# Optimization experiments

Measured on AMD Instinct MI355X. Metric: run time of the kernel, lower is better.

## Reference

```python
import jax, jax.numpy as jnp
import numpy as np

B, L, D, FF = 4, 4096, 1024, 4096
EPS = 1e-06


def setup_inputs() -> dict:
    key = jax.random.key(0)
    ks = jax.random.split(key, 20)
    s_d = 1.0 / np.sqrt(D)
    s_ff = 1.0 / np.sqrt(FF)
    inp = {
        "x": jax.random.normal(ks[0], (B, L, D), jnp.float32),
        "hidden": jax.random.normal(ks[1], (B, D), jnp.float32),
        # sioconv linears (stored as [in, out])
        "w_ln_z": jax.random.normal(ks[2], (D, D), jnp.float32) * s_d,
        "b_ln_z": jnp.zeros((D,), jnp.float32),
        "w_dt": jax.random.normal(ks[3], (D, D), jnp.float32) * s_d,
        "b_dt": jnp.zeros((D,), jnp.float32),
        "w_y": jax.random.normal(ks[4], (D, D), jnp.float32) * s_d,
        "b_y": jnp.zeros((D,), jnp.float32),
        "w_y_act": jax.random.normal(ks[5], (D, D), jnp.float32) * s_d,
        "b_y_act": jnp.zeros((D,), jnp.float32),
        # FFN SwiGLU
        "w_fc": jax.random.normal(ks[6], (D, FF), jnp.float32) * s_d,
        "b_fc": jnp.zeros((FF,), jnp.float32),
        "w_fc_act": jax.random.normal(ks[7], (D, FF), jnp.float32) * s_d,
        "b_fc_act": jnp.zeros((FF,), jnp.float32),
        "w_out": jax.random.normal(ks[8], (FF, D), jnp.float32) * s_ff,
        "b_out": jnp.zeros((D,), jnp.float32),
        # RMSNorm gains
        "g_sio": jnp.ones((D,), jnp.float32),
        "g_ffn": jnp.ones((D,), jnp.float32),
    }
    return inp


def _rmsnorm(x, g):
    return x * jax.lax.rsqrt(jnp.mean(x * x, axis=-1, keepdims=True) + EPS) * g


def _sioconv(x, hidden, w_ln_z, b_ln_z, w_dt, b_dt, w_y, b_y, w_y_act, b_y_act):
    # x: [B,L,D], hidden: [B,D]
    ln_z = -jax.nn.softplus(-(x @ w_ln_z + b_ln_z))       # [B,L,D]
    dt = x @ w_dt + b_dt
    ln_da = -jax.nn.softplus(-dt)
    ln_o_da = -jax.nn.softplus(dt)
    ln_o_da_cumsum = jnp.cumsum(ln_o_da, axis=1)
    # inner-chunk: exp(logcumsumexp(ln_z + ln_da - cumsum) + cumsum)
    lse = jax.lax.cumlogsumexp(ln_z + ln_da - ln_o_da_cumsum, axis=1)
    h_inner = jnp.exp(lse + ln_o_da_cumsum)
    # cross-chunk: decay applied to incoming hidden state
    h_cross = jnp.exp(ln_o_da_cumsum) * hidden[:, None, :]
    h = h_inner + h_cross
    y = (h @ w_y + b_y) * jax.nn.silu(x @ w_y_act + b_y_act)
    return y, h


def _ffn(x, w_fc, b_fc, w_fc_act, b_fc_act, w_out, b_out):
    return (x @ w_fc + b_fc) * jax.nn.silu(x @ w_fc_act + b_fc_act) @ w_out + b_out


def reference(x, hidden, w_ln_z, b_ln_z, w_dt, b_dt, w_y, b_y, w_y_act, b_y_act,
              w_fc, b_fc, w_fc_act, b_fc_act, w_out, b_out, g_sio, g_ffn):
    x_res = x
    y, h = _sioconv(_rmsnorm(x, g_sio), hidden,
                    w_ln_z, b_ln_z, w_dt, b_dt, w_y, b_y, w_y_act, b_y_act)
    x = y + x_res  # dropout is identity (p=0 / eval)
    x_res = x
    x = _ffn(_rmsnorm(x, g_ffn), w_fc, b_fc, w_fc_act, b_fc_act, w_out, b_out) + x_res
    return (x, h)
```

## Files before the change

### kernel.cpp

```cpp
#include <hip/hip_runtime.h>
#include <stdint.h>

using u16 = unsigned short;
typedef __attribute__((ext_vector_type(8))) __bf16 bf16x8;
typedef __attribute__((ext_vector_type(4))) float f32x4;

#define DEV __device__ __forceinline__

static constexpr int kB = 4, kL = 4096, kD = 1024, kFF = 4096;
static constexpr int kM = kB * kL;
static constexpr int kLC = 256, kNC = kL / kLC;
static constexpr float kEPS = 1e-6f;

DEV u16 f2bf(float v) {
  union { float f; uint32_t u; } x; x.f = v;
  uint32_t r = x.u + 0x7FFFu + ((x.u >> 16) & 1u);
  return (u16)(r >> 16);
}
DEV float bf2f(u16 u) {
  union { uint32_t u; float f; } x; x.u = (uint32_t)u << 16; return x.f;
}
DEV float sigm(float x) { return 1.0f / (1.0f + __expf(-x)); }

DEV void gload_lds16(const void* g, void* l) {
  __builtin_amdgcn_global_load_lds(
      (const __attribute__((address_space(1))) void*)g,
      (__attribute__((address_space(3))) void*)l, 16, 0, 0);
}

__global__ __launch_bounds__(256) void wtrans_all(
    const float* __restrict__ w_ln_z, const float* __restrict__ w_dt,
    const float* __restrict__ w_fca, const float* __restrict__ w_fc,
    const float* __restrict__ w_yact, const float* __restrict__ w_y,
    const float* __restrict__ w_out_,
    u16* __restrict__ wzdT, u16* __restrict__ wfgT, u16* __restrict__ wyaT,
    u16* __restrict__ wyT, u16* __restrict__ woutT) {
  const int bid = blockIdx.x;
  const float *a, *b; u16* out; int K, Ncols, bx, local; bool pair;
  if (bid < 2048)       { local = bid;         a = w_ln_z; b = w_dt; out = wzdT;  K = 1024; Ncols = 1024; bx = 64;  pair = true;  }
  else if (bid < 10240) { local = bid - 2048;  a = w_fca;  b = w_fc; out = wfgT;  K = 1024; Ncols = 4096; bx = 256; pair = true;  }
  else if (bid < 11264) { local = bid - 10240; a = w_yact; b = nullptr; out = wyaT; K = 1024; Ncols = 1024; bx = 32; pair = false; }
  else if (bid < 12288) { local = bid - 11264; a = w_y;    b = nullptr; out = wyT;  K = 1024; Ncols = 1024; bx = 32; pair = false; }
  else                  { local = bid - 12288; a = w_out_; b = nullptr; out = woutT; K = 4096; Ncols = 1024; bx = 32; pair = false; }
  const int n0 = (local % bx) * 32, k0 = (local / bx) * 32;
  __shared__ float t[32][33];
  const int tx = threadIdx.x, ty = threadIdx.y;
  const float* src; int c0;
  if (pair) { src = ((n0 >> 5) & 1) ? b : a; c0 = (n0 >> 6) * 32; }
  else      { src = a; c0 = n0; }
#pragma unroll
  for (int i = 0; i < 4; ++i)
    t[ty + i * 8][tx] = src[(size_t)(k0 + ty + i * 8) * Ncols + (c0 + tx)];
  __syncthreads();
#pragma unroll
  for (int i = 0; i < 4; ++i)
    out[(size_t)(n0 + ty + i * 8) * K + (k0 + tx)] = f2bf(t[tx][ty + i * 8]);
}

__global__ __launch_bounds__(256) void rmsnorm_kernel(const float* __restrict__ x,
                                                      const float* __restrict__ g,
                                                      u16* __restrict__ out) {
  const int row = blockIdx.x;
  const int t = threadIdx.x;
  const float4 v = ((const float4*)(x + (size_t)row * kD))[t];
  float ss = v.x * v.x + v.y * v.y + v.z * v.z + v.w * v.w;
#pragma unroll
  for (int o = 1; o < 64; o <<= 1) ss += __shfl_xor(ss, o, 64);
  __shared__ float red[4];
  if ((t & 63) == 0) red[t >> 6] = ss;
  __syncthreads();
  const float tot = red[0] + red[1] + red[2] + red[3];
  const float sc = rsqrtf(tot * (1.0f / kD) + kEPS);
  const float4 gv = ((const float4*)g)[t];
  const uint32_t lo = (uint32_t)f2bf(v.x * sc * gv.x) | ((uint32_t)f2bf(v.y * sc * gv.y) << 16);
  const uint32_t hi = (uint32_t)f2bf(v.z * sc * gv.z) | ((uint32_t)f2bf(v.w * sc * gv.w) << 16);
  *(uint2*)(out + (size_t)row * kD + t * 4) = make_uint2(lo, hi);
}

__global__ __launch_bounds__(256) void rmsnorm_b16(const u16* __restrict__ x,
                                                   const float* __restrict__ g,
                                                   u16* __restrict__ out) {
  const int row = blockIdx.x;
  const int t = threadIdx.x;
  const uint2 raw = ((const uint2*)(x + (size_t)row * kD))[t];
  const float v0 = bf2f((u16)(raw.x & 0xffff)), v1 = bf2f((u16)(raw.x >> 16));
  const float v2 = bf2f((u16)(raw.y & 0xffff)), v3 = bf2f((u16)(raw.y >> 16));
  float ss = v0 * v0 + v1 * v1 + v2 * v2 + v3 * v3;
#pragma unroll
  for (int o = 1; o < 64; o <<= 1) ss += __shfl_xor(ss, o, 64);
  __shared__ float red[4];
  if ((t & 63) == 0) red[t >> 6] = ss;
  __syncthreads();
  const float tot = red[0] + red[1] + red[2] + red[3];
  const float sc = rsqrtf(tot * (1.0f / kD) + kEPS);
  const float4 gv = ((const float4*)g)[t];
  const uint32_t lo = (uint32_t)f2bf(v0 * sc * gv.x) | ((uint32_t)f2bf(v1 * sc * gv.y) << 16);
  const uint32_t hi = (uint32_t)f2bf(v2 * sc * gv.z) | ((uint32_t)f2bf(v3 * sc * gv.w) << 16);
  *(uint2*)(out + (size_t)row * kD + t * 4) = make_uint2(lo, hi);
}

template <int MODE>
__global__ __launch_bounds__(512) void gemm256(
    const u16* __restrict__ A, const u16* __restrict__ Bt,
    const float* __restrict__ bias, const float* __restrict__ bias2,
    const u16* __restrict__ aux, int auxld,
    const float* __restrict__ res, float* __restrict__ Cf,
    u16* __restrict__ Cb, u16* __restrict__ C2b,
    float* __restrict__ Pg, float* __restrict__ Sg,
    int M, int N, int K) {
  __shared__ u16 sm[65536];
  const int tid = threadIdx.x;
  const int lane = tid & 63;
  const int wave = tid >> 6;
  const int wr = wave >> 2, wc = wave & 3;

  const int gx = gridDim.x;
  const int nwg = gx * gridDim.y;
  const int bid = blockIdx.y * gx + blockIdx.x;
  const int q = nwg >> 3, r = nwg & 7;
  const int xcd = bid & 7, idx0 = bid >> 3;
  const int wg = (xcd < r ? xcd * (q + 1) : r * (q + 1) + (xcd - r) * q) + idx0;
  const int m0 = (wg / gx) * 256, n0 = (wg % gx) * 256;

  const int NK = K >> 6;

  const int l8 = lane >> 3, l7 = lane & 7;
  const int rsub = wave * 8 + l8;
  const int kel = (l7 ^ l8) * 8;
  const size_t srcA = (size_t)(m0 + rsub) * K + kel;
  const size_t srcB = (size_t)(n0 + rsub) * K + kel;

  auto stage_half = [&](int kt, int half) {
    const int bsel = (kt & 1) * 32768;
    if (half < 2) {
      u16* d = sm + bsel + tid * 8 + half * 8192;
      const u16* s = A + srcA + (size_t)kt * 64 + (size_t)(half * 2) * 64 * K;
      gload_lds16(s, d);
      gload_lds16(s + (size_t)64 * K, d + 4096);
    } else {
      const int hh = half - 2;
      u16* d = sm + bsel + 16384 + tid * 8 + hh * 8192;
      const u16* s = Bt + srcB + (size_t)kt * 64 + (size_t)(hh * 2) * 64 * K;
      gload_lds16(s, d);
      gload_lds16(s + (size_t)64 * K, d + 4096);
    }
  };

  const int ra = lane & 15;
  const int kx0 = ((lane >> 4) ^ l7) * 8;
  const int kx1 = (((lane >> 4) + 4) ^ l7) * 8;

  f32x4 acc[8][4] = {};
  bf16x8 al[4][2], ah[4][2], bl[2][2], bh[2][2];

  stage_half(0, 0); stage_half(0, 1); stage_half(0, 2); stage_half(0, 3);
  stage_half(1, 0);
  asm volatile("s_waitcnt vmcnt(2)");
  asm volatile("s_barrier" ::: "memory");

  for (int h = 0; h < NK; ++h) {
    const u16* as = sm + (h & 1) * 32768 + (wr * 128 + ra) * 64;
    const u16* bs = sm + (h & 1) * 32768 + 16384 + (wc * 64 + ra) * 64;

#pragma unroll
    for (int mi = 0; mi < 4; ++mi) {
      al[mi][0] = *(const bf16x8*)(as + mi * 16 * 64 + kx0);
      al[mi][1] = *(const bf16x8*)(as + mi * 16 * 64 + kx1);
    }
#pragma unroll
    for (int ni = 0; ni < 2; ++ni) {
      bl[ni][0] = *(const bf16x8*)(bs + ni * 16 * 64 + kx0);
      bl[ni][1] = *(const bf16x8*)(bs + ni * 16 * 64 + kx1);
    }
    if (h + 1 < NK) stage_half(h + 1, 1);
    asm volatile("s_barrier" ::: "memory");
    asm volatile("s_waitcnt lgkmcnt(0)");
    __builtin_amdgcn_s_setprio(1);
#pragma unroll
    for (int mi = 0; mi < 4; ++mi)
#pragma unroll
      for (int ni = 0; ni < 2; ++ni)
#pragma unroll
        for (int kk = 0; kk < 2; ++kk)
          acc[mi][ni] = __builtin_amdgcn_mfma_f32_16x16x32_bf16(al[mi][kk], bl[ni][kk], acc[mi][ni], 0, 0, 0);
    __builtin_amdgcn_s_setprio(0);
    asm volatile("s_barrier" ::: "memory");

#pragma unroll
    for (int ni = 0; ni < 2; ++ni) {
      bh[ni][0] = *(const bf16x8*)(bs + (32 + ni * 16) * 64 + kx0);
      bh[ni][1] = *(const bf16x8*)(bs + (32 + ni * 16) * 64 + kx1);
    }
    if (h + 1 < NK) stage_half(h + 1, 2);
    asm volatile("s_barrier" ::: "memory");
    asm volatile("s_waitcnt lgkmcnt(0)");
    __builtin_amdgcn_s_setprio(1);
#pragma unroll
    for (int mi = 0; mi < 4; ++mi)
#pragma unroll
      for (int ni = 0; ni < 2; ++ni)
#pragma unroll
        for (int kk = 0; kk < 2; ++kk)
          acc[mi][2 + ni] = __builtin_amdgcn_mfma_f32_16x16x32_bf16(al[mi][kk], bh[ni][kk], acc[mi][2 + ni], 0, 0, 0);
    __builtin_amdgcn_s_setprio(0);
    asm volatile("s_barrier" ::: "memory");

#pragma unroll
    for (int mi = 0; mi < 4; ++mi) {
      ah[mi][0] = *(const bf16x8*)(as + (64 + mi * 16) * 64 + kx0);
      ah[mi][1] = *(const bf16x8*)(as + (64 + mi * 16) * 64 + kx1);
    }
    if (h + 1 < NK) stage_half(h + 1, 3);
    asm volatile("s_barrier" ::: "memory");
    asm volatile("s_waitcnt lgkmcnt(0)");
    __builtin_amdgcn_s_setprio(1);
#pragma unroll
    for (int mi = 0; mi < 4; ++mi)
#pragma unroll
      for (int ni = 0; ni < 2; ++ni)
#pragma unroll
        for (int kk = 0; kk < 2; ++kk)
          acc[4 + mi][ni] = __builtin_amdgcn_mfma_f32_16x16x32_bf16(ah[mi][kk], bl[ni][kk], acc[4 + mi][ni], 0, 0, 0);
    __builtin_amdgcn_s_setprio(0);
    asm volatile("s_barrier" ::: "memory");

    if (h + 2 < NK) stage_half(h + 2, 0);
    asm volatile("s_barrier" ::: "memory");
    __builtin_amdgcn_s_setprio(1);
#pragma unroll
    for (int mi = 0; mi < 4; ++mi)
#pragma unroll
      for (int ni = 0; ni < 2; ++ni)
#pragma unroll
        for (int kk = 0; kk < 2; ++kk)
          acc[4 + mi][2 + ni] = __builtin_amdgcn_mfma_f32_16x16x32_bf16(ah[mi][kk], bh[ni][kk], acc[4 + mi][2 + ni], 0, 0, 0);
    __builtin_amdgcn_s_setprio(0);
    if (h + 2 < NK) asm volatile("s_waitcnt vmcnt(2)");
    else            asm volatile("s_waitcnt vmcnt(0)");
    asm volatile("s_barrier" ::: "memory");
  }

  const int ca = ra;
  const int rq = (lane >> 4) * 4;
  if (MODE == 7) {
    const int Nout = N >> 1;
    float Pacc[2] = {1.f, 1.f}, Sacc[2] = {0.f, 0.f};
#pragma unroll
    for (int mi = 0; mi < 8; ++mi) {
#pragma unroll
      for (int ni = 0; ni < 2; ++ni) {
        const int cout = (n0 >> 1) + wc * 32 + ni * 16 + ca;
        const float b1 = bias[cout], b2 = bias2[cout];
        float pj = 1.f, sj = 0.f;
#pragma unroll
        for (int j = 0; j < 4; ++j) {
          const int rr = m0 + wr * 128 + mi * 16 + rq + j;
          const size_t idx = (size_t)rr * Nout + cout;
          const float v1 = acc[mi][ni][j] + b1;
          const float v2 = acc[mi][2 + ni][j] + b2;
          const float Aa = sigm(-v2);
          const float Bb = sigm(v1) * sigm(v2);
          Cf[idx] = Aa;
          C2b[idx] = f2bf(Bb);
          pj *= Aa;
          sj = fmaf(Aa, sj, Bb);
        }
        float P16 = 1.f, S16 = 0.f;
#pragma unroll
        for (int qq = 0; qq < 4; ++qq) {
          const float pq = __shfl(pj, ca + qq * 16, 64);
          const float sq = __shfl(sj, ca + qq * 16, 64);
          P16 *= pq;
          S16 = fmaf(pq, S16, sq);
        }
        Sacc[ni] = fmaf(P16, Sacc[ni], S16);
        Pacc[ni] *= P16;
      }
    }
    float* smF = (float*)sm;
    __syncthreads();
    if ((lane >> 4) == 0) {
#pragma unroll
      for (int ni = 0; ni < 2; ++ni) {
        const int col = wc * 32 + ni * 16 + ca;
        smF[wr * 128 + col] = Pacc[ni];
        smF[256 + wr * 128 + col] = Sacc[ni];
      }
    }
    __syncthreads();
    if (wr == 0 && (lane >> 4) == 0) {
      const int bb = m0 >> 12, cc = (m0 & 4095) >> 8;
#pragma unroll
      for (int ni = 0; ni < 2; ++ni) {
        const int col = wc * 32 + ni * 16 + ca;
        const float P0 = smF[col],       P1 = smF[128 + col];
        const float S0 = smF[256 + col], S1 = smF[256 + 128 + col];
        const size_t o = ((size_t)bb * kNC + cc) * kD + ((n0 >> 1) + col);
        Pg[o] = P0 * P1;
        Sg[o] = fmaf(P1, S0, S1);
      }
    }
  } else {
#pragma unroll
    for (int mi = 0; mi < 8; ++mi) {
#pragma unroll
      for (int ni = 0; ni < 4; ++ni) {
        const int c = n0 + wc * 64 + ni * 16 + ca;
        const float bz = bias[c];
#pragma unroll
        for (int j = 0; j < 4; ++j) {
          const int rr = m0 + wr * 128 + mi * 16 + rq + j;
          const size_t idx = (size_t)rr * N + c;
          const float v = acc[mi][ni][j] + bz;
          if (MODE == 2) {
            const float a = bf2f(aux[(size_t)rr * auxld + c]);
            Cb[idx] = f2bf(v * (a * sigm(a)) + res[idx]);
          } else if (MODE == 8) {
            Cf[idx] = v + bf2f(aux[(size_t)rr * auxld + c]);
          } else {
            Cb[idx] = f2bf(v);
          }
        }
      }
    }
  }
}

__global__ __launch_bounds__(512, 4) void gemm_ffn(
    const u16* __restrict__ A, const u16* __restrict__ Bt,
    const float* __restrict__ bias, const float* __restrict__ bias2,
    u16* __restrict__ Cb, int M, int N, int K) {
  __shared__ u16 sm[24576];
  const int tid = threadIdx.x;
  const int lane = tid & 63;
  const int wave = tid >> 6;
  const int wr = wave >> 1, wc = wave & 1;

  const int gx = gridDim.x;
  const int nwg = gx * gridDim.y;
  const int bid = blockIdx.y * gx + blockIdx.x;
  const int q = nwg >> 3, r = nwg & 7;
  const int xcd = bid & 7, idx0 = bid >> 3;
  const int wg = (xcd < r ? xcd * (q + 1) : r * (q + 1) + (xcd - r) * q) + idx0;
  const int per = gridDim.y * 4;
  const int sg = wg / per, srem = wg % per;
  const int m0 = (srem >> 2) * 256;
  const int n0 = (sg * 4 + (srem & 3)) * 128;

  const int NK = K >> 5;

  const int rsub = wave * 16 + (lane >> 2);
  const int kel = ((lane & 3) ^ ((lane >> 3) & 3)) * 8;
  const size_t srcA = (size_t)(m0 + rsub) * K + kel;
  const size_t srcB = (size_t)(n0 + rsub) * K + kel;

  auto stageA = [&](int kt) {
    u16* d = sm + (kt & 1) * 12288 + tid * 8;
    const u16* s = A + srcA + (size_t)kt * 32;
    gload_lds16(s, d);
    gload_lds16(s + (size_t)128 * K, d + 4096);
  };
  auto stageB = [&](int kt) {
    gload_lds16(Bt + srcB + (size_t)kt * 32,
                sm + (kt & 1) * 12288 + 8192 + tid * 8);
  };

  const int ra = lane & 15;
  const int rb = ra * 32 + ((((lane >> 4) ^ (ra >> 1)) & 3) << 3);

  f32x4 acc[4][4] = {};
  bf16x8 af[4], bfr[4];

  stageA(0); stageB(0);
  if (NK > 1) { stageA(1); stageB(1); }
  asm volatile("s_waitcnt vmcnt(3)");
  asm volatile("s_barrier" ::: "memory");

  for (int h = 0; h < NK; ++h) {
    const u16* Az = sm + (h & 1) * 12288 + wr * 2048;
    const u16* Bz = sm + (h & 1) * 12288 + 8192 + wc * 2048;

#pragma unroll
    for (int mi = 0; mi < 4; ++mi) af[mi] = *(const bf16x8*)(Az + mi * 512 + rb);
    bfr[0] = *(const bf16x8*)(Bz + rb);
    bfr[1] = *(const bf16x8*)(Bz + 512 + rb);
    asm volatile("s_barrier" ::: "memory");
    asm volatile("s_waitcnt lgkmcnt(0)");
    __builtin_amdgcn_s_setprio(1);
#pragma unroll
    for (int mi = 0; mi < 4; ++mi)
#pragma unroll
      for (int ni = 0; ni < 2; ++ni)
        acc[mi][ni] = __builtin_amdgcn_mfma_f32_16x16x32_bf16(af[mi], bfr[ni], acc[mi][ni], 0, 0, 0);
    __builtin_amdgcn_s_setprio(0);
    asm volatile("s_barrier" ::: "memory");

    bfr[2] = *(const bf16x8*)(Bz + 1024 + rb);
    bfr[3] = *(const bf16x8*)(Bz + 1536 + rb);
    if (h + 2 < NK) stageA(h + 2);
    asm volatile("s_barrier" ::: "memory");
    asm volatile("s_waitcnt lgkmcnt(0)");
    __builtin_amdgcn_s_setprio(1);
#pragma unroll
    for (int mi = 0; mi < 4; ++mi)
      acc[mi][2] = __builtin_amdgcn_mfma_f32_16x16x32_bf16(af[mi], bfr[2], acc[mi][2], 0, 0, 0);
    __builtin_amdgcn_s_setprio(0);
    asm volatile("s_barrier" ::: "memory");

    if (h + 2 < NK) stageB(h + 2);
    __builtin_amdgcn_s_setprio(1);
#pragma unroll
    for (int mi = 0; mi < 4; ++mi)
      acc[mi][3] = __builtin_amdgcn_mfma_f32_16x16x32_bf16(af[mi], bfr[3], acc[mi][3], 0, 0, 0);
    __builtin_amdgcn_s_setprio(0);
    if (h + 2 < NK) asm volatile("s_waitcnt vmcnt(3)");
    else            asm volatile("s_waitcnt vmcnt(0)");
    asm volatile("s_barrier" ::: "memory");
  }

  const int ca = lane & 15;
  const int rq = (lane >> 4) * 4;
  const int Nout = N >> 1;
#pragma unroll
  for (int mi = 0; mi < 4; ++mi) {
#pragma unroll
    for (int ni = 0; ni < 2; ++ni) {
      const int cout = (n0 >> 1) + wc * 32 + ni * 16 + ca;
      const float b1 = bias[cout], b2 = bias2[cout];
#pragma unroll
      for (int j = 0; j < 4; ++j) {
        const int rr = m0 + wr * 64 + mi * 16 + rq + j;
        const size_t idx = (size_t)rr * Nout + cout;
        const float v1 = acc[mi][ni][j] + b1;
        const float v2 = acc[mi][2 + ni][j] + b2;
        Cb[idx] = f2bf(v2 * (v1 * sigm(v1)));
      }
    }
  }
}

__global__ __launch_bounds__(256) void scan_phase2(const float* __restrict__ P,
                                                   const float* __restrict__ S,
                                                   const float* __restrict__ hidden,
                                                   float* __restrict__ Hini) {
  const int d = blockIdx.x * 256 + threadIdx.x;
  const int b = blockIdx.y;
  float carry = hidden[(size_t)b * kD + d];
  for (int c = 0; c < kNC; ++c) {
    const size_t o = ((size_t)b * kNC + c) * kD + d;
    Hini[o] = carry;
    carry = fmaf(P[o], carry, S[o]);
  }
}

__global__ __launch_bounds__(256) void scan_phase3(const float* __restrict__ Aa,
                                                   const u16* __restrict__ Bv,
                                                   const float* __restrict__ Hini,
                                                   float* __restrict__ Hout,
                                                   u16* __restrict__ Hbf) {
  const int d = blockIdx.x * 256 + threadIdx.x;
  const int c = blockIdx.y, b = blockIdx.z;
  float h = Hini[((size_t)b * kNC + c) * kD + d];
  size_t base = ((size_t)b * kL + (size_t)c * kLC) * kD + d;
#pragma unroll 4
  for (int l = 0; l < kLC; ++l) {
    h = fmaf(Aa[base], h, bf2f(Bv[base]));
    Hout[base] = h;
    Hbf[base] = f2bf(h);
    base += kD;
  }
}

extern "C" void kernel_launch(void* const* d_in, const int* in_sizes, int n_in,
                              void* d_out, int out_size, void* d_ws, size_t ws_size,
                              hipStream_t stream) {
  const float* x      = (const float*)d_in[0];
  const float* hidden = (const float*)d_in[1];
  const float* w_ln_z = (const float*)d_in[2];
  const float* b_ln_z = (const float*)d_in[3];
  const float* w_dt   = (const float*)d_in[4];
  const float* b_dt   = (const float*)d_in[5];
  const float* w_y    = (const float*)d_in[6];
  const float* b_y    = (const float*)d_in[7];
  const float* w_yact = (const float*)d_in[8];
  const float* b_yact = (const float*)d_in[9];
  const float* w_fc   = (const float*)d_in[10];
  const float* b_fc   = (const float*)d_in[11];
  const float* w_fca  = (const float*)d_in[12];
  const float* b_fca  = (const float*)d_in[13];
  const float* w_out  = (const float*)d_in[14];
  const float* b_out  = (const float*)d_in[15];
  const float* g_sio  = (const float*)d_in[16];
  const float* g_ffn  = (const float*)d_in[17];

  char* ws = (char*)d_ws;
  const size_t MiB = 1ull << 20;
  u16* wzdT  = (u16*)(ws + 0 * MiB);
  u16* wyaT  = (u16*)(ws + 4 * MiB);
  u16* wyT   = (u16*)(ws + 6 * MiB);
  u16* wfgT  = (u16*)(ws + 8 * MiB);
  u16* woutT = (u16*)(ws + 24 * MiB);
  u16*   xn    = (u16*)(ws + 33 * MiB);
  u16*   yabuf = (u16*)(ws + 65 * MiB);
  float* Abuf  = (float*)(ws + 97 * MiB);
  u16*   x1b   = (u16*)(ws + 97 * MiB);
  u16*   Bvbuf = (u16*)(ws + 161 * MiB);
  u16*   hbf   = (u16*)(ws + 225 * MiB);
  u16*   Ubuf  = (u16*)(ws + 161 * MiB);
  float* Pbuf  = (float*)(ws + 289 * MiB);
  float* Sbuf  = (float*)(ws + 290 * MiB);
  float* Hini  = (float*)(ws + 291 * MiB);

  float* xout = (float*)d_out;
  float* hout = xout + (size_t)kM * kD;

  wtrans_all<<<16384, dim3(32, 8), 0, stream>>>(
      w_ln_z, w_dt, w_fca, w_fc, w_yact, w_y, w_out,
      wzdT, wfgT, wyaT, wyT, woutT);

  rmsnorm_kernel<<<kM, 256, 0, stream>>>(x, g_sio, xn);

  gemm256<7><<<dim3(2048 / 256, kM / 256), 512, 0, stream>>>(
      xn, wzdT, b_ln_z, b_dt, nullptr, 0, nullptr, Abuf, nullptr, Bvbuf,
      Pbuf, Sbuf, kM, 2048, kD);
  gemm256<5><<<dim3(kD / 256, kM / 256), 512, 0, stream>>>(
      xn, wyaT, b_yact, nullptr, nullptr, 0, nullptr, nullptr, yabuf, nullptr,
      nullptr, nullptr, kM, kD, kD);

  scan_phase2<<<dim3(kD / 256, kB), 256, 0, stream>>>(Pbuf, Sbuf, hidden, Hini);
  scan_phase3<<<dim3(kD / 256, kNC, kB), 256, 0, stream>>>(Abuf, Bvbuf, Hini, hout, hbf);

  gemm256<2><<<dim3(kD / 256, kM / 256), 512, 0, stream>>>(
      hbf, wyT, b_y, nullptr, yabuf, kD, x, nullptr, x1b, nullptr,
      nullptr, nullptr, kM, kD, kD);

  rmsnorm_b16<<<kM, 256, 0, stream>>>(x1b, g_ffn, xn);

  gemm_ffn<<<dim3(8192 / 128, kM / 256), 512, 0, stream>>>(
      xn, wfgT, b_fca, b_fc, Ubuf, kM, 8192, kD);

  gemm256<8><<<dim3(kD / 256, kM / 256), 512, 0, stream>>>(
      Ubuf, woutT, b_out, nullptr, x1b, kD, nullptr, xout, nullptr, nullptr,
      nullptr, nullptr, kM, kD, kFF);
}
```

Baseline: 730.6 us.

## Enlarge FFN gate GEMM tile to 256x256 with BK=64 and 8-wave 2x4 layout

Replaces the 256x128, BK=32 FFN up/gate GEMM with a 256x256, BK=64 tile. It uses a 2x4 wave grid, a new XOR swizzle and a four-part staged double buffer with 128KB of LDS. Each wave now holds an 8x4 accumulator array, which doubles the reuse of every A and B fragment and halves the number of K iterations and barriers per FLOP. The cost is much higher register and LDS use, dropping occupancy to roughly one block per CU, and a simpler tile mapping that no longer groups N tiles for L2 locality.

```diff
diff --git a/kernel.cpp b/kernel.cpp
--- a/kernel.cpp
+++ b/kernel.cpp
@@ -326,15 +326,15 @@
   }
 }
 
-__global__ __launch_bounds__(512, 4) void gemm_ffn(
+__global__ __launch_bounds__(512) void gemm_ffn8(
     const u16* __restrict__ A, const u16* __restrict__ Bt,
     const float* __restrict__ bias, const float* __restrict__ bias2,
     u16* __restrict__ Cb, int M, int N, int K) {
-  __shared__ u16 sm[24576];
+  __shared__ u16 sm[65536];
   const int tid = threadIdx.x;
   const int lane = tid & 63;
   const int wave = tid >> 6;
-  const int wr = wave >> 1, wc = wave & 1;
+  const int wr = wave >> 2, wc = wave & 3;
 
   const int gx = gridDim.x;
   const int nwg = gx * gridDim.y;
@@ -342,48 +342,64 @@
   const int q = nwg >> 3, r = nwg & 7;
   const int xcd = bid & 7, idx0 = bid >> 3;
   const int wg = (xcd < r ? xcd * (q + 1) : r * (q + 1) + (xcd - r) * q) + idx0;
-  const int per = gridDim.y * 4;
-  const int sg = wg / per, srem = wg % per;
-  const int m0 = (srem >> 2) * 256;
-  const int n0 = (sg * 4 + (srem & 3)) * 128;
-
-  const int NK = K >> 5;
-
-  const int rsub = wave * 16 + (lane >> 2);
-  const int kel = ((lane & 3) ^ ((lane >> 3) & 3)) * 8;
+  const int m0 = (wg / gx) * 256, n0 = (wg % gx) * 256;
+
+  const int NK = K >> 6;
+
+  const int l8 = lane >> 3, l7 = lane & 7;
+  const int rsub = wave * 8 + l8;
+  const int kel = (l7 ^ l8) * 8;
   const size_t srcA = (size_t)(m0 + rsub) * K + kel;
   const size_t srcB = (size_t)(n0 + rsub) * K + kel;
 
-  auto stageA = [&](int kt) {
-    u16* d = sm + (kt & 1) * 12288 + tid * 8;
-    const u16* s = A + srcA + (size_t)kt * 32;
-    gload_lds16(s, d);
-    gload_lds16(s + (size_t)128 * K, d + 4096);
+  auto stage_half = [&](int kt, int half) {
+    const int bsel = (kt & 1) * 32768;
+    if (half < 2) {
+      u16* d = sm + bsel + tid * 8 + half * 8192;
+      const u16* s = A + srcA + (size_t)kt * 64 + (size_t)(half * 2) * 64 * K;
+      gload_lds16(s, d);
+      gload_lds16(s + (size_t)64 * K, d + 4096);
+    } else {
+      const int hh = half - 2;
+      u16* d = sm + bsel + 16384 + tid * 8 + hh * 8192;
+      const u16* s = Bt + srcB + (size_t)kt * 64 + (size_t)(hh * 2) * 64 * K;
+      gload_lds16(s, d);
+      gload_lds16(s + (size_t)64 * K, d + 4096);
+    }
   };
-  auto stageB = [&](int kt) {
-    gload_lds16(Bt + srcB + (size_t)kt * 32,
-                sm + (kt & 1) * 12288 + 8192 + tid * 8);
-  };
 
   const int ra = lane & 15;
-  const int rb = ra * 32 + ((((lane >> 4) ^ (ra >> 1)) & 3) << 3);
-
-  f32x4 acc[4][4] = {};
-  bf16x8 af[4], bfr[4];
-
-  stageA(0); stageB(0);
-  if (NK > 1) { stageA(1); stageB(1); }
-  asm volatile("s_waitcnt vmcnt(3)");
+  const int kx0 = ((lane >> 4) ^ l7) * 8;
+  const int kx1 = (((lane >> 4) + 4) ^ l7) * 8;
+
+  f32x4 acc[8][4] = {};
+  bf16x8 al[4][2], ah[4][2], bl[2][2], bh[2][2];
+
+  stage_half(0, 0); stage_half(0, 1); stage_half(0, 2); stage_half(0, 3);
+  if (NK > 1) {
+    stage_half(1, 2); stage_half(1, 3);
+    asm volatile("s_waitcnt vmcnt(4)");
+  } else {
+    asm volatile("s_waitcnt vmcnt(0)");
+  }
   asm volatile("s_barrier" ::: "memory");
 
-  for (int h = 0; h < NK; ++h) {
-    const u16* Az = sm + (h & 1) * 12288 + wr * 2048;
-    const u16* Bz = sm + (h & 1) * 12288 + 8192 + wc * 2048;
-
-#pragma unroll
-    for (int mi = 0; mi < 4; ++mi) af[mi] = *(const bf16x8*)(Az + mi * 512 + rb);
-    bfr[0] = *(const bf16x8*)(Bz + rb);
-    bfr[1] = *(const bf16x8*)(Bz + 512 + rb);
+  for (int s = 0; s < NK; ++s) {
+    const int bsel = (s & 1) * 32768;
+    const u16* as = sm + bsel + (wr * 128 + ra) * 64;
+    const u16* bs = sm + bsel + 16384 + (wc * 64 + ra) * 64;
+
+#pragma unroll
+    for (int mi = 0; mi < 4; ++mi) {
+      al[mi][0] = *(const bf16x8*)(as + mi * 16 * 64 + kx0);
+      al[mi][1] = *(const bf16x8*)(as + mi * 16 * 64 + kx1);
+    }
+#pragma unroll
+    for (int ni = 0; ni < 2; ++ni) {
+      bl[ni][0] = *(const bf16x8*)(bs + ni * 16 * 64 + kx0);
+      bl[ni][1] = *(const bf16x8*)(bs + ni * 16 * 64 + kx1);
+    }
+    if (s + 1 < NK) stage_half(s + 1, 0);
     asm volatile("s_barrier" ::: "memory");
     asm volatile("s_waitcnt lgkmcnt(0)");
     __builtin_amdgcn_s_setprio(1);
@@ -391,45 +407,78 @@
     for (int mi = 0; mi < 4; ++mi)
 #pragma unroll
       for (int ni = 0; ni < 2; ++ni)
-        acc[mi][ni] = __builtin_amdgcn_mfma_f32_16x16x32_bf16(af[mi], bfr[ni], acc[mi][ni], 0, 0, 0);
-    __builtin_amdgcn_s_setprio(0);
-    asm volatile("s_barrier" ::: "memory");
-
-    bfr[2] = *(const bf16x8*)(Bz + 1024 + rb);
-    bfr[3] = *(const bf16x8*)(Bz + 1536 + rb);
-    if (h + 2 < NK) stageA(h + 2);
+#pragma unroll
+        for (int kk = 0; kk < 2; ++kk)
+          acc[mi][ni] = __builtin_amdgcn_mfma_f32_16x16x32_bf16(al[mi][kk], bl[ni][kk], acc[mi][ni], 0, 0, 0);
+    __builtin_amdgcn_s_setprio(0);
+    asm volatile("s_barrier" ::: "memory");
+
+#pragma unroll
+    for (int ni = 0; ni < 2; ++ni) {
+      bh[ni][0] = *(const bf16x8*)(bs + (32 + ni * 16) * 64 + kx0);
+      bh[ni][1] = *(const bf16x8*)(bs + (32 + ni * 16) * 64 + kx1);
+    }
+    if (s + 1 < NK) stage_half(s + 1, 1);
     asm volatile("s_barrier" ::: "memory");
     asm volatile("s_waitcnt lgkmcnt(0)");
     __builtin_amdgcn_s_setprio(1);
 #pragma unroll
     for (int mi = 0; mi < 4; ++mi)
-      acc[mi][2] = __builtin_amdgcn_mfma_f32_16x16x32_bf16(af[mi], bfr[2], acc[mi][2], 0, 0, 0);
-    __builtin_amdgcn_s_setprio(0);
-    asm volatile("s_barrier" ::: "memory");
-
-    if (h + 2 < NK) stageB(h + 2);
-    __builtin_amdgcn_s_setprio(1);
-#pragma unroll
-    for (int mi = 0; mi < 4; ++mi)
-      acc[mi][3] = __builtin_amdgcn_mfma_f32_16x16x32_bf16(af[mi], bfr[3], acc[mi][3], 0, 0, 0);
-    __builtin_amdgcn_s_setprio(0);
-    if (h + 2 < NK) asm volatile("s_waitcnt vmcnt(3)");
+#pragma unroll
+      for (int ni = 0; ni < 2; ++ni)
+#pragma unroll
+        for (int kk = 0; kk < 2; ++kk)
+          acc[mi][2 + ni] = __builtin_amdgcn_mfma_f32_16x16x32_bf16(al[mi][kk], bh[ni][kk], acc[mi][2 + ni], 0, 0, 0);
+    __builtin_amdgcn_s_setprio(0);
+    asm volatile("s_barrier" ::: "memory");
+
+#pragma unroll
+    for (int mi = 0; mi < 4; ++mi) {
+      ah[mi][0] = *(const bf16x8*)(as + (64 + mi * 16) * 64 + kx0);
+      ah[mi][1] = *(const bf16x8*)(as + (64 + mi * 16) * 64 + kx1);
+    }
+    if (s + 2 < NK) stage_half(s + 2, 2);
+    asm volatile("s_barrier" ::: "memory");
+    asm volatile("s_waitcnt lgkmcnt(0)");
+    __builtin_amdgcn_s_setprio(1);
+#pragma unroll
+    for (int mi = 0; mi < 4; ++mi)
+#pragma unroll
+      for (int ni = 0; ni < 2; ++ni)
+#pragma unroll
+        for (int kk = 0; kk < 2; ++kk)
+          acc[4 + mi][ni] = __builtin_amdgcn_mfma_f32_16x16x32_bf16(ah[mi][kk], bl[ni][kk], acc[4 + mi][ni], 0, 0, 0);
+    __builtin_amdgcn_s_setprio(0);
+    asm volatile("s_barrier" ::: "memory");
+
+    if (s + 2 < NK) stage_half(s + 2, 3);
+    asm volatile("s_barrier" ::: "memory");
+    __builtin_amdgcn_s_setprio(1);
+#pragma unroll
+    for (int mi = 0; mi < 4; ++mi)
+#pragma unroll
+      for (int ni = 0; ni < 2; ++ni)
+#pragma unroll
+        for (int kk = 0; kk < 2; ++kk)
+          acc[4 + mi][2 + ni] = __builtin_amdgcn_mfma_f32_16x16x32_bf16(ah[mi][kk], bh[ni][kk], acc[4 + mi][2 + ni], 0, 0, 0);
+    __builtin_amdgcn_s_setprio(0);
+    if (s + 2 < NK) asm volatile("s_waitcnt vmcnt(4)");
     else            asm volatile("s_waitcnt vmcnt(0)");
     asm volatile("s_barrier" ::: "memory");
   }
 
-  const int ca = lane & 15;
+  const int ca = ra;
   const int rq = (lane >> 4) * 4;
   const int Nout = N >> 1;
 #pragma unroll
-  for (int mi = 0; mi < 4; ++mi) {
+  for (int mi = 0; mi < 8; ++mi) {
 #pragma unroll
     for (int ni = 0; ni < 2; ++ni) {
       const int cout = (n0 >> 1) + wc * 32 + ni * 16 + ca;
       const float b1 = bias[cout], b2 = bias2[cout];
 #pragma unroll
       for (int j = 0; j < 4; ++j) {
-        const int rr = m0 + wr * 64 + mi * 16 + rq + j;
+        const int rr = m0 + wr * 128 + mi * 16 + rq + j;
         const size_t idx = (size_t)rr * Nout + cout;
         const float v1 = acc[mi][ni][j] + b1;
         const float v2 = acc[mi][2 + ni][j] + b2;
@@ -536,7 +585,7 @@
 
   rmsnorm_b16<<<kM, 256, 0, stream>>>(x1b, g_ffn, xn);
 
-  gemm_ffn<<<dim3(8192 / 128, kM / 256), 512, 0, stream>>>(
+  gemm_ffn8<<<dim3(8192 / 256, kM / 256), 512, 0, stream>>>(
       xn, wfgT, b_fca, b_fc, Ubuf, kM, 8192, kD);
 
   gemm256<8><<<dim3(kD / 256, kM / 256), 512, 0, stream>>>(
```

Result: no change. 725.6 us (-0.7%).
